# Kernel optimization log

Hardware: AMD Instinct MI355X
Metric: run time of the kernel (lower is better)

The kernel has to match this reference:

```python
import jax, jax.numpy as jnp
import numpy as np

B, S, E, ND = 4, 2048, 1024, 2


def setup_inputs() -> dict:
    key = jax.random.key(0)
    ks = jax.random.split(key, 10)
    def lin_w(k, out_f, in_f):
        return (jax.random.normal(k, (out_f, in_f), jnp.float32) / np.sqrt(in_f).astype(np.float32))
    inp = {}
    inp["x"] = jax.random.normal(ks[0], (B, S, E), jnp.float32)
    inp["tfidf_scores"] = jax.random.uniform(ks[1], (B, S), jnp.float32)
    names = ["q_f", "k_f", "v_f", "q_b", "k_b", "v_b"]
    for i, n in enumerate(names):
        inp["W" + n] = lin_w(ks[2 + i], ND * E, E)
        inp["b" + n] = jnp.zeros((ND * E,), jnp.float32)
    inp["Wo"] = lin_w(ks[8], E, ND * E)
    inp["bo"] = jnp.zeros((E,), jnp.float32)
    return inp


def _proj(x, W, b):
    # Linear(E -> ND*E) then reshape to (B, S, ND, E)
    y = jnp.einsum('bse,fe->bsf', x, W) + b
    return y.reshape(x.shape[0], x.shape[1], ND, E)


def _attend(q, k, v, tfidf):
    # q,k,v: (B, S, ND, E); tfidf: (B, S) weights keys
    scale = 1.0 / jnp.sqrt(jnp.asarray(E, q.dtype))
    scores = jnp.einsum('bsde,btde->bdst', q, k) * scale
    scores = scores * tfidf[:, None, None, :]
    attn = jax.nn.softmax(scores, axis=-1)
    return jnp.einsum('bdst,btde->bsde', attn, v)


def reference(x, tfidf_scores, Wq_f, bq_f, Wk_f, bk_f, Wv_f, bv_f,
              Wq_b, bq_b, Wk_b, bk_b, Wv_b, bv_b, Wo, bo):
    # forward direction
    qf = _proj(x, Wq_f, bq_f)
    kf = _proj(x, Wk_f, bk_f)
    vf = _proj(x, Wv_f, bv_f)
    out_f = _attend(qf, kf, vf, tfidf_scores)
    # backward direction: reversed sequence
    xr = x[:, ::-1]
    tr = tfidf_scores[:, ::-1]
    qb = _proj(xr, Wq_b, bq_b)
    kb = _proj(xr, Wk_b, bk_b)
    vb = _proj(xr, Wv_b, bv_b)
    out_b = _attend(qb, kb, vb, tr)[:, ::-1]
    comb = (out_f + out_b).reshape(x.shape[0], x.shape[1], ND * E)
    return jnp.einsum('bsf,ef->bse', comb, Wo) + bo
```

## Files before the change

### kernel.cpp

```cpp
#include <hip/hip_runtime.h>
#include <hip/hip_bf16.h>
#include <stdint.h>

#define SEQ 2048
#define EMB 1024

typedef __attribute__((ext_vector_type(4))) float f32x4;
typedef __attribute__((ext_vector_type(8))) __bf16 bf16x8v;
typedef __attribute__((ext_vector_type(8))) unsigned short u16x8;
typedef __attribute__((ext_vector_type(4))) unsigned short u16x4;

static __device__ __forceinline__ float bf2f(unsigned short u){
  union { unsigned int i; float f; } v; v.i = ((unsigned int)u) << 16; return v.f;
}
static __device__ __forceinline__ unsigned short f2bf(float f){
  union { float f; unsigned int i; } v; v.f = f;
  unsigned int r = v.i + 0x7FFFu + ((v.i >> 16) & 1u);
  return (unsigned short)(r >> 16);
}

static __device__ __forceinline__ void gload16(const unsigned short* g, unsigned short* l){
  __builtin_amdgcn_global_load_lds(
      (__attribute__((address_space(1))) unsigned int*)(g),
      (__attribute__((address_space(3))) unsigned int*)(l), 16, 0, 0);
}

static __device__ __forceinline__ int xcd_swz(int bid, int nwg){
  int q = nwg >> 3;
  return (bid & 7) * q + (bid >> 3);
}

__global__ __launch_bounds__(256) void k_cvt_bf16(const float* __restrict__ in,
                                                  unsigned short* __restrict__ out, long n4){
  long i = (long)blockIdx.x * 256 + threadIdx.x;
  if (i >= n4) return;
  float4 v = ((const float4*)in)[i];
  u16x4 o; o.x = f2bf(v.x); o.y = f2bf(v.y); o.z = f2bf(v.z); o.w = f2bf(v.w);
  ((u16x4*)out)[i] = o;
}

__global__ __launch_bounds__(256) void k_build_wcat(
    const float* __restrict__ w0, const float* __restrict__ w1,
    const float* __restrict__ w2, const float* __restrict__ w3,
    const float* __restrict__ w4, const float* __restrict__ w5,
    unsigned short* __restrict__ wcat){
  long i = (long)blockIdx.x * 256 + threadIdx.x;
  long g = i * 4;
  int m = (int)(g >> 21);
  const float* src = (m==0)?w0:(m==1)?w1:(m==2)?w2:(m==3)?w3:(m==4)?w4:w5;
  long loc = g & ((1L<<21)-1);
  float4 v = *(const float4*)&src[loc];
  u16x4 o; o.x=f2bf(v.x); o.y=f2bf(v.y); o.z=f2bf(v.z); o.w=f2bf(v.w);
  *(u16x4*)&wcat[g] = o;
}

__global__ __launch_bounds__(256) void k_build_bcat(
    const float* b0, const float* b1, const float* b2,
    const float* b3, const float* b4, const float* b5, float* __restrict__ bcat){
  int i = blockIdx.x * 256 + threadIdx.x;
  int m = i >> 11;
  const float* src = (m==0)?b0:(m==1)?b1:(m==2)?b2:(m==3)?b3:(m==4)?b4:b5;
  bcat[i] = src[i & 2047];
}

#define M_LIN   0
#define M_SCORE 1
#define M_PV    2
#define M_OUT   3

template<int MODE, int BN>
__global__ __launch_bounds__(512, 2)
void gemm4p(const unsigned short* __restrict__ A_,
            const unsigned short* __restrict__ B_,
            unsigned short* __restrict__ Cb, float* __restrict__ Cf,
            const float* __restrict__ bias, const float* __restrict__ tfb,
            int ld, int ldc, int tilesN, int accflag)
{
  constexpr int KD  = (MODE==M_PV || MODE==M_OUT) ? 2048 : 1024;
  constexpr int NT  = KD/64;
  constexpr int NREP= BN/64;
  constexpr int NLO = NREP/2;
  constexpr int LB  = BN/128;

  __shared__ __attribute__((aligned(16))) unsigned short As[2][256*64];
  __shared__ __attribute__((aligned(16))) unsigned short Bs[2][BN*64];

  const int tid = threadIdx.x;
  const int lane = tid & 63, wid = tid >> 6;
  const int wr = wid >> 2, wc = wid & 3;

  const int tile = xcd_swz(blockIdx.x, gridDim.x);
  const int tm = tile / tilesN, tn = tile % tilesN;
  const int y  = blockIdx.y;

  const unsigned short *A0 = A_, *B0 = B_;
  unsigned short* Cbp = Cb;
  float* Cfp = Cf;
  float* rsp = nullptr;
  const float* trow = nullptr;
  const float* rsd = nullptr;

  if constexpr (MODE==M_SCORE) {
    const int bl = y >> 1, d = y & 1;
    A0 = A_ + (size_t)bl*SEQ*ld + (size_t)blockIdx.z*6144 + d*1024;
    B0 = A0 + 2048;
    Cbp = Cb + ((size_t)blockIdx.z*gridDim.y + y)*SEQ*SEQ;
    rsp = Cf + ((size_t)blockIdx.z*gridDim.y + y)*SEQ;
    trow = tfb + (size_t)bl*SEQ;
  } else if constexpr (MODE==M_PV) {
    A0 = A_ + (size_t)y*SEQ*SEQ;
    B0 = B_ + (size_t)y*EMB*SEQ;
    Cbp = Cb + (size_t)(y>>1)*SEQ*2048 + (y&1)*1024;
    rsd = tfb + (size_t)y*SEQ;
  }

  const int sr = tid >> 3, ss = tid & 7;
  const int swz = (ss ^ (sr & 7)) * 8;
  const long tmrow = (long)tm*256, tncol = (long)tn*BN;
  const int lrow = lane & 15, lks = lane >> 4;

  const unsigned short* gA = A0 + (size_t)(tmrow + sr)*ld + swz;
  const unsigned short* gB = B0 + (size_t)(tncol + sr)*ld + swz;

  f32x4 acc[8][NREP];
  #pragma unroll
  for (int m=0;m<8;++m)
    #pragma unroll
    for (int n=0;n<NREP;++n)
      #pragma unroll
      for (int r=0;r<4;++r) acc[m][n][r] = 0.f;

#define SA_H(b_, h_, t_) { \
    const long ko_ = (long)(t_)*64; \
    _Pragma("unroll") \
    for (int p=0;p<2;++p){ \
      const int p2_ = (h_)*2 + p; \
      gload16(gA + (size_t)(p2_*64)*ld + ko_, &As[b_][p2_*4096 + tid*8]); \
    } }

#define SB_H(b_, h_, t_) { \
    const long ko_ = (long)(t_)*64; \
    _Pragma("unroll") \
    for (int p=0;p<LB;++p){ \
      const int p2_ = (h_)*LB + p; \
      gload16(gB + (size_t)(p2_*64)*ld + ko_, &Bs[b_][p2_*4096 + tid*8]); \
    } }

#define LDA_F(dst, b_, mh) { \
    _Pragma("unroll") \
    for (int m=0;m<4;++m){ \
      int row_ = (m + 4*(mh))*32 + wr*16 + lrow; \
      _Pragma("unroll") \
      for (int kk=0;kk<2;++kk){ \
        int slot_ = (kk*4 + lks) ^ (row_ & 7); \
        dst[m*2+kk] = *(const bf16x8v*)&As[b_][row_*64 + slot_*8]; \
      } } }

#define LDB_F(dst, b_, nh) { \
    _Pragma("unroll") \
    for (int n=0;n<NLO;++n){ \
      int row_ = (n + NLO*(nh))*64 + wc*16 + lrow; \
      _Pragma("unroll") \
      for (int kk=0;kk<2;++kk){ \
        int slot_ = (kk*4 + lks) ^ (row_ & 7); \
        dst[n*2+kk] = *(const bf16x8v*)&Bs[b_][row_*64 + slot_*8]; \
      } } }

#define MMAC(mh, bfrag, nh) { \
    __builtin_amdgcn_s_setprio(1); \
    _Pragma("unroll") \
    for (int m=0;m<4;++m) \
      _Pragma("unroll") \
      for (int n=0;n<NLO;++n) \
        _Pragma("unroll") \
        for (int kk=0;kk<2;++kk) \
          acc[(mh)*4+m][(nh)*NLO+n] = __builtin_amdgcn_mfma_f32_16x16x32_bf16( \
              aF[m*2+kk], bfrag[n*2+kk], acc[(mh)*4+m][(nh)*NLO+n], 0,0,0); \
    __builtin_amdgcn_s_setprio(0); }

#define GATEN(N_) { \
    asm volatile("s_waitcnt vmcnt(" #N_ ")" ::: "memory"); \
    __builtin_amdgcn_sched_barrier(0); \
    __builtin_amdgcn_s_barrier(); \
    __builtin_amdgcn_sched_barrier(0); }

#define SBAR() __builtin_amdgcn_sched_barrier(0);

  bf16x8v aF[8], bL[2*NLO], bH[2*NLO];

  SA_H(0,0,0); SB_H(0,0,0); SB_H(0,1,0); SA_H(0,1,0);
  if constexpr (LB==2) { GATEN(4) } else { GATEN(3) }
  LDA_F(aF, 0, 0);
  LDB_F(bL, 0, 0);
  SBAR()

  for (int t = 0; t < NT-1; ++t) {
    const int b_ = t & 1, nb_ = b_ ^ 1;
    SA_H(nb_,0,t+1);
    GATEN(4)
    LDB_F(bH, b_, 1);
    SBAR()
    MMAC(0, bL, 0);
    SB_H(nb_,0,t+1);
    if constexpr (LB==2) { GATEN(4) } else { GATEN(3) }
    MMAC(0, bH, 1);
    LDA_F(aF, b_, 1);
    SBAR()
    SB_H(nb_,1,t+1);
    MMAC(1, bH, 1);
    SA_H(nb_,1,t+1);
    if constexpr (LB==2) { GATEN(4) } else { GATEN(3) }
    MMAC(1, bL, 0);
    LDA_F(aF, nb_, 0);
    LDB_F(bL, nb_, 0);
    SBAR()
  }

  {
    const int b_ = (NT-1) & 1;
    GATEN(2)
    LDB_F(bH, b_, 1);
    SBAR()
    MMAC(0, bL, 0);
    GATEN(0)
    MMAC(0, bH, 1);
    LDA_F(aF, b_, 1);
    SBAR()
    MMAC(1, bH, 1);
    MMAC(1, bL, 0);
  }

  const int rr = (lane >> 4) * 4, cc = lane & 15;

  if constexpr (MODE==M_SCORE) {
    float cm[NREP];
    #pragma unroll
    for (int n=0;n<NREP;++n) cm[n] = 0.03125f * trow[tncol + n*64 + wc*16 + cc];
    #pragma unroll
    for (int m=0;m<8;++m)
      #pragma unroll
      for (int n=0;n<NREP;++n)
        #pragma unroll
        for (int r=0;r<4;++r)
          acc[m][n][r] = __expf(acc[m][n][r] * cm[n]);
    #pragma unroll
    for (int n=0;n<NREP;++n){
      const long col = tncol + n*64 + wc*16 + cc;
      #pragma unroll
      for (int m=0;m<8;++m){
        const long row = tmrow + m*32 + wr*16 + rr;
        #pragma unroll
        for (int r=0;r<4;++r)
          Cbp[(row + r)*(size_t)ldc + col] = f2bf(acc[m][n][r]);
      }
    }
    #pragma unroll
    for (int m=0;m<8;++m){
      #pragma unroll
      for (int r=0;r<4;++r){
        float s = 0.f;
        #pragma unroll
        for (int n=0;n<NREP;++n) s += acc[m][n][r];
        s += __shfl_xor(s, 1); s += __shfl_xor(s, 2);
        s += __shfl_xor(s, 4); s += __shfl_xor(s, 8);
        if ((lane & 15) == 0)
          atomicAdd(&rsp[tmrow + m*32 + wr*16 + rr + r], s);
      }
    }
  } else if constexpr (MODE==M_PV) {
    #pragma unroll
    for (int m=0;m<8;++m){
      const long row0 = tmrow + m*32 + wr*16 + rr;
      float4 rsv = *(const float4*)&rsd[row0];
      float inv[4];
      inv[0] = 1.f/rsv.x; inv[1] = 1.f/rsv.y; inv[2] = 1.f/rsv.z; inv[3] = 1.f/rsv.w;
      #pragma unroll
      for (int n=0;n<NREP;++n){
        const long col = tncol + n*64 + wc*16 + cc;
        #pragma unroll
        for (int r=0;r<4;++r){
          size_t idx = (row0 + r)*(size_t)ldc + col;
          float w = acc[m][n][r]*inv[r] + (accflag ? bf2f(Cbp[idx]) : 0.f);
          Cbp[idx] = f2bf(w);
        }
      }
    }
  } else {
    #pragma unroll
    for (int n=0;n<NREP;++n){
      const long col = tncol + n*64 + wc*16 + cc;
      const float cadd = bias[col];
      #pragma unroll
      for (int m=0;m<8;++m){
        const long row = tmrow + m*32 + wr*16 + rr;
        #pragma unroll
        for (int r=0;r<4;++r){
          float v = acc[m][n][r] + cadd;
          if constexpr (MODE==M_OUT) Cfp[(row + r)*(size_t)ldc + col] = v;
          else                       Cbp[(row + r)*(size_t)ldc + col] = f2bf(v);
        }
      }
    }
  }
#undef SA_H
#undef SB_H
#undef LDA_F
#undef LDB_F
#undef MMAC
#undef GATEN
#undef SBAR
}

__global__ __launch_bounds__(256) void k_transpose_v(const unsigned short* __restrict__ Vsrc,
                                                     unsigned short* __restrict__ VT, int ld){
  __shared__ unsigned short tile[64][72];
  int yo = blockIdx.z*gridDim.y + blockIdx.y;
  int bl = blockIdx.y >> 1, d = blockIdx.y & 1;
  int tt = (blockIdx.x & 31) * 64;
  int te = (blockIdx.x >> 5) * 64;
  const unsigned short* src = Vsrc + (size_t)bl*SEQ*ld + (size_t)blockIdx.z*6144 + d*1024;
  int tid = threadIdx.x;
  #pragma unroll
  for (int it=0; it<2; ++it){
    int c = it*256 + tid;
    int r = c >> 3, c8 = (c & 7) * 8;
    u16x8 v = *(const u16x8*)&src[(size_t)(tt + r)*ld + te + c8];
    *(u16x8*)&tile[r][c8] = v;
  }
  __syncthreads();
  #pragma unroll
  for (int it=0; it<2; ++it){
    int c = it*256 + tid;
    int re = c >> 3, c8 = (c & 7) * 8;
    u16x8 o;
    #pragma unroll
    for (int j=0;j<8;++j) o[j] = tile[c8 + j][re];
    *(u16x8*)&VT[((size_t)yo*EMB + te + re)*SEQ + tt + c8] = o;
  }
}

extern "C" void kernel_launch(void* const* d_in, const int* in_sizes, int n_in,
                              void* d_out, int out_size, void* d_ws, size_t ws_size,
                              hipStream_t stream){
  const float* x  = (const float*)d_in[0];
  const float* tf = (const float*)d_in[1];
  const float* W[6]; const float* bz[6];
  for (int i=0;i<6;++i){ W[i]=(const float*)d_in[2+2*i]; bz[i]=(const float*)d_in[3+2*i]; }
  const float* Wo = (const float*)d_in[14];
  const float* bo = (const float*)d_in[15];
  float* outp = (float*)d_out;

  auto al = [](size_t b){ return (b + 255) & ~(size_t)255; };
  const size_t SZ_XB   = (size_t)8192*1024*2;
  const size_t SZ_WCAT = (size_t)12288*1024*2;
  const size_t SZ_WOB  = (size_t)1024*2048*2;
  const size_t SZ_BCAT = (size_t)12288*4;
  const size_t SZ_AO   = (size_t)8192*2048*2;
  const size_t fixedB  = al(SZ_XB)+al(SZ_WCAT)+al(SZ_WOB)+al(SZ_BCAT)+al(SZ_AO);

  auto chB = [&](int CB, bool merged, bool both)->size_t {
    int nd = both ? 2 : 1;
    return al((size_t)CB*SEQ*(merged?12288:6144)*2)
         + al((size_t)nd*CB*2*SEQ*SEQ*2)
         + al((size_t)nd*CB*2*EMB*SEQ*2)
         + al((size_t)nd*CB*2*SEQ*4);
  };
  int CB; bool merged, both;
  if      (ws_size >= fixedB + chB(4,true ,true )) { CB=4; merged=true;  both=true;  }
  else if (ws_size >= fixedB + chB(2,true ,true )) { CB=2; merged=true;  both=true;  }
  else if (ws_size >= fixedB + chB(2,true ,false)) { CB=2; merged=true;  both=false; }
  else if (ws_size >= fixedB + chB(2,false,false)) { CB=2; merged=false; both=false; }
  else if (ws_size >= fixedB + chB(1,false,false)) { CB=1; merged=false; both=false; }
  else return;
  const int ldY = merged ? 12288 : 6144;
  const int nd = both ? 2 : 1;

  char* ws = (char*)d_ws; size_t off = 0;
  auto take = [&](size_t bytes)->char* { char* p = ws + off; off += al(bytes); return p; };
  unsigned short* xb   = (unsigned short*)take(SZ_XB);
  unsigned short* Wcat = (unsigned short*)take(SZ_WCAT);
  unsigned short* WoB  = (unsigned short*)take(SZ_WOB);
  float*          bcat = (float*)take(SZ_BCAT);
  unsigned short* AO   = (unsigned short*)take(SZ_AO);
  unsigned short* Ych  = (unsigned short*)take((size_t)CB*SEQ*ldY*2);
  const size_t scHalf = (size_t)CB*2*SEQ*SEQ;
  const size_t vtHalf = (size_t)CB*2*EMB*SEQ;
  const size_t rsHalf = (size_t)CB*2*SEQ;
  unsigned short* Sc = (unsigned short*)take(nd*scHalf*2);
  unsigned short* VT = (unsigned short*)take(nd*vtHalf*2);
  float*          rs = (float*)take(nd*rsHalf*4);

  k_cvt_bf16   <<<8192, 256, 0, stream>>>(x, xb, 2097152);
  k_build_wcat <<<12288,256, 0, stream>>>(W[0],W[1],W[2],W[3],W[4],W[5], Wcat);
  k_cvt_bf16   <<<2048, 256, 0, stream>>>(Wo, WoB, 524288);
  k_build_bcat <<<48,   256, 0, stream>>>(bz[0],bz[1],bz[2],bz[3],bz[4],bz[5], bcat);

  for (int c = 0; c < 4/CB; ++c) {
    const int b0 = c*CB;
    const unsigned short* xchunk = xb + (size_t)b0*SEQ*1024;
    if (merged) {
      gemm4p<M_LIN,256><<<dim3(CB*8*48, 1), 512, 0, stream>>>(
          xchunk, Wcat, Ych, nullptr, bcat, nullptr, 1024, 12288, 48, 0);
    }
    if (both) {
      hipMemsetAsync(rs, 0, 2*rsHalf*4, stream);
      gemm4p<M_SCORE,256><<<dim3(64, 2*CB, 2), 512, 0, stream>>>(
          Ych, nullptr, Sc, rs, nullptr, tf + (size_t)b0*SEQ, ldY, 2048, 8, 0);
      k_transpose_v<<<dim3(512, 2*CB, 2), 256, 0, stream>>>(Ych + 4096, VT, ldY);
      for (int dir = 0; dir < 2; ++dir) {
        gemm4p<M_PV,128><<<dim3(64, 2*CB), 512, 0, stream>>>(
            Sc + dir*scHalf, VT + dir*vtHalf, AO + (size_t)b0*SEQ*2048, nullptr,
            nullptr, rs + dir*rsHalf, 2048, 2048, 8, dir);
      }
    } else {
      for (int dir = 0; dir < 2; ++dir) {
        const unsigned short* Ybase = Ych + (merged ? dir*6144 : 0);
        if (!merged) {
          gemm4p<M_LIN,256><<<dim3(CB*8*24, 1), 512, 0, stream>>>(
              xchunk, Wcat + (size_t)dir*6144*1024, Ych, nullptr,
              bcat + dir*6144, nullptr, 1024, 6144, 24, 0);
        }
        hipMemsetAsync(rs, 0, rsHalf*4, stream);
        gemm4p<M_SCORE,256><<<dim3(64, 2*CB, 1), 512, 0, stream>>>(
            Ybase, nullptr, Sc, rs, nullptr, tf + (size_t)b0*SEQ, ldY, 2048, 8, 0);
        k_transpose_v<<<dim3(512, 2*CB, 1), 256, 0, stream>>>(Ybase + 4096, VT, ldY);
        gemm4p<M_PV,128><<<dim3(64, 2*CB), 512, 0, stream>>>(
            Sc, VT, AO + (size_t)b0*SEQ*2048, nullptr,
            nullptr, rs, 2048, 2048, 8, dir);
      }
    }
  }
  gemm4p<M_OUT,128><<<dim3(256, 1), 512, 0, stream>>>(
      AO, WoB, nullptr, outp, bo, nullptr, 2048, 1024, 8, 0);
}
```

Baseline: 705.5 us.

## Fuse V transpose into projection GEMM epilogue and switch to column-major tile order

The projection GEMM epilogue now writes V columns straight into the transposed VT buffer when both directions are merged, so the separate transpose kernel launch is dropped. Tile indexing changes from row-major to M-fastest order, which alters how blocks share A and B tiles in cache. The saving is one launch plus a full read and write of V. In exchange, the epilogue stores are strided with 8-byte writes along the sequence, and the non-merged path still uses the old transpose kernel.

```diff
diff --git a/kernel.cpp b/kernel.cpp
--- a/kernel.cpp
+++ b/kernel.cpp
@@ -74,7 +74,8 @@
             const unsigned short* __restrict__ B_,
             unsigned short* __restrict__ Cb, float* __restrict__ Cf,
             const float* __restrict__ bias, const float* __restrict__ tfb,
-            int ld, int ldc, int tilesN, int accflag)
+            unsigned short* __restrict__ vtp, int nbl,
+            int ld, int ldc, int tilesM, int accflag)
 {
   constexpr int KD  = (MODE==M_PV || MODE==M_OUT) ? 2048 : 1024;
   constexpr int NT  = KD/64;
@@ -90,7 +91,7 @@
   const int wr = wid >> 2, wc = wid & 3;
 
   const int tile = xcd_swz(blockIdx.x, gridDim.x);
-  const int tm = tile / tilesN, tn = tile % tilesN;
+  const int tm = tile % tilesM, tn = tile / tilesM;
   const int y  = blockIdx.y;
 
   const unsigned short *A0 = A_, *B0 = B_;
@@ -285,6 +286,44 @@
         }
       }
     }
+  } else if constexpr (MODE==M_LIN) {
+    const bool vt_tile = (vtp != nullptr) && ((tncol % 6144) >= 4096);
+    if (vt_tile) {
+      const int dir = (int)(tncol / 6144);
+      const int bl  = (int)(tmrow >> 11);
+      const long vrel0 = (tncol % 6144) - 4096;
+      unsigned short* vbase = vtp + (size_t)dir*nbl*2*EMB*SEQ;
+      #pragma unroll
+      for (int n=0;n<NREP;++n){
+        const long col = tncol + n*64 + wc*16 + cc;
+        const float cadd = bias[col];
+        const long ef = vrel0 + n*64 + wc*16 + cc;
+        const int d = (int)(ef >> 10);
+        const long e = ef & 1023;
+        unsigned short* vrow = vbase + ((size_t)(bl*2 + d)*EMB + e)*SEQ;
+        #pragma unroll
+        for (int m=0;m<8;++m){
+          const long t0 = tmrow + m*32 + wr*16 + rr;
+          u16x4 o;
+          #pragma unroll
+          for (int r=0;r<4;++r) o[r] = f2bf(acc[m][n][r] + cadd);
+          *(u16x4*)&vrow[(t0 & 2047)] = o;
+        }
+      }
+    } else {
+      #pragma unroll
+      for (int n=0;n<NREP;++n){
+        const long col = tncol + n*64 + wc*16 + cc;
+        const float cadd = bias[col];
+        #pragma unroll
+        for (int m=0;m<8;++m){
+          const long row = tmrow + m*32 + wr*16 + rr;
+          #pragma unroll
+          for (int r=0;r<4;++r)
+            Cbp[(row + r)*(size_t)ldc + col] = f2bf(acc[m][n][r] + cadd);
+        }
+      }
+    }
   } else {
     #pragma unroll
     for (int n=0;n<NREP;++n){
@@ -294,11 +333,8 @@
       for (int m=0;m<8;++m){
         const long row = tmrow + m*32 + wr*16 + rr;
         #pragma unroll
-        for (int r=0;r<4;++r){
-          float v = acc[m][n][r] + cadd;
-          if constexpr (MODE==M_OUT) Cfp[(row + r)*(size_t)ldc + col] = v;
-          else                       Cbp[(row + r)*(size_t)ldc + col] = f2bf(v);
-        }
+        for (int r=0;r<4;++r)
+          Cfp[(row + r)*(size_t)ldc + col] = acc[m][n][r] + cadd;
       }
     }
   }
@@ -400,17 +436,18 @@
     const unsigned short* xchunk = xb + (size_t)b0*SEQ*1024;
     if (merged) {
       gemm4p<M_LIN,256><<<dim3(CB*8*48, 1), 512, 0, stream>>>(
-          xchunk, Wcat, Ych, nullptr, bcat, nullptr, 1024, 12288, 48, 0);
+          xchunk, Wcat, Ych, nullptr, bcat, nullptr,
+          both ? VT : nullptr, CB, 1024, 12288, CB*8, 0);
     }
     if (both) {
       hipMemsetAsync(rs, 0, 2*rsHalf*4, stream);
       gemm4p<M_SCORE,256><<<dim3(64, 2*CB, 2), 512, 0, stream>>>(
-          Ych, nullptr, Sc, rs, nullptr, tf + (size_t)b0*SEQ, ldY, 2048, 8, 0);
-      k_transpose_v<<<dim3(512, 2*CB, 2), 256, 0, stream>>>(Ych + 4096, VT, ldY);
+          Ych, nullptr, Sc, rs, nullptr, tf + (size_t)b0*SEQ,
+          nullptr, 0, ldY, 2048, 8, 0);
       for (int dir = 0; dir < 2; ++dir) {
         gemm4p<M_PV,128><<<dim3(64, 2*CB), 512, 0, stream>>>(
             Sc + dir*scHalf, VT + dir*vtHalf, AO + (size_t)b0*SEQ*2048, nullptr,
-            nullptr, rs + dir*rsHalf, 2048, 2048, 8, dir);
+            nullptr, rs + dir*rsHalf, nullptr, 0, 2048, 2048, 8, dir);
       }
     } else {
       for (int dir = 0; dir < 2; ++dir) {
@@ -418,18 +455,19 @@
         if (!merged) {
           gemm4p<M_LIN,256><<<dim3(CB*8*24, 1), 512, 0, stream>>>(
               xchunk, Wcat + (size_t)dir*6144*1024, Ych, nullptr,
-              bcat + dir*6144, nullptr, 1024, 6144, 24, 0);
+              bcat + dir*6144, nullptr, nullptr, 0, 1024, 6144, CB*8, 0);
         }
         hipMemsetAsync(rs, 0, rsHalf*4, stream);
         gemm4p<M_SCORE,256><<<dim3(64, 2*CB, 1), 512, 0, stream>>>(
-            Ybase, nullptr, Sc, rs, nullptr, tf + (size_t)b0*SEQ, ldY, 2048, 8, 0);
+            Ybase, nullptr, Sc, rs, nullptr, tf + (size_t)b0*SEQ,
+            nullptr, 0, ldY, 2048, 8, 0);
         k_transpose_v<<<dim3(512, 2*CB, 1), 256, 0, stream>>>(Ybase + 4096, VT, ldY);
         gemm4p<M_PV,128><<<dim3(64, 2*CB), 512, 0, stream>>>(
             Sc, VT, AO + (size_t)b0*SEQ*2048, nullptr,
-            nullptr, rs, 2048, 2048, 8, dir);
+            nullptr, rs, nullptr, 0, 2048, 2048, 8, dir);
       }
     }
   }
   gemm4p<M_OUT,128><<<dim3(256, 1), 512, 0, stream>>>(
-      AO, WoB, nullptr, outp, bo, nullptr, 2048, 1024, 8, 0);
-}
+      AO, WoB, nullptr, outp, bo, nullptr, nullptr, 0, 2048, 1024, 32, 0);
+}
```

After: 727.2 us. 1.03x slower.
